# Kernel tuning notes

Hardware: AMD Instinct MI355X
Metric: run time of the kernel (lower is better)

Reference implementation:

```python
import jax, jax.numpy as jnp
import numpy as np

VOCAB_SIZE = 50000

def setup_inputs() -> dict:
    key = jax.random.key(0)
    # token index sequences: [batch, seq_len], values in [0, vocab)
    x = jax.random.randint(key, (2048, 200), 0, VOCAB_SIZE, dtype=jnp.int64)
    return {"x": x}

def reference(x) -> jnp.ndarray:
    # Faithful to: sum_{l} one_hot(x[b, l], V)  ->  [batch, vocab] count histogram.
    # Implemented as a scatter-add instead of materializing the
    # [batch, seq_len, vocab] one-hot tensor (same math, O(B*L) traffic on the
    # index side plus the [B, V] output).
    B, L = x.shape
    rows = jnp.broadcast_to(jnp.arange(B)[:, None], (B, L))  # [B, L]
    out = jnp.zeros((B, VOCAB_SIZE), dtype=jnp.float32)
    out = out.at[rows, x].add(jnp.float32(1.0))
    return out
```

## Files before the change

kernel.cpp:

```cpp
#include <hip/hip_runtime.h>
#include <hip/hip_bf16.h>

#define VOCAB 50000
#define SEQ   200
#define NDW   (VOCAB / 4)
#define NV4   (VOCAB / 16)

__global__ __launch_bounds__(256) void MultihotEmbedding_16458314678493_kernel(
    const int* __restrict__ x, float* __restrict__ out) {
  __shared__ unsigned cnt[NDW];

  uint4* __restrict__ c4 = (uint4*)cnt;
  const uint4 z = make_uint4(0u, 0u, 0u, 0u);
  for (int i = threadIdx.x; i < NV4; i += 256) c4[i] = z;
  __syncthreads();

  const int row = blockIdx.x;
  const int* __restrict__ xr = x + row * SEQ;
  for (int t = threadIdx.x; t < SEQ; t += 256) {
    const int idx = xr[t];
    atomicAdd(&cnt[idx >> 2], 1u << ((idx & 3) * 8));
  }
  __syncthreads();

  float4* __restrict__ o4 = (float4*)(out + (size_t)row * VOCAB);
  for (int i = threadIdx.x; i < NDW; i += 256) {
    const unsigned u = cnt[i];
    float4 v;
    v.x = (float)(u & 0xffu);
    v.y = (float)((u >> 8) & 0xffu);
    v.z = (float)((u >> 16) & 0xffu);
    v.w = (float)(u >> 24);
    o4[i] = v;
  }
}

extern "C" void kernel_launch(void* const* d_in, const int* in_sizes, int n_in,
                              void* d_out, int out_size, void* d_ws, size_t ws_size,
                              hipStream_t stream) {
  const int* x = (const int*)d_in[0];
  float* out = (float*)d_out;
  const int batch = in_sizes[0] / SEQ;
  MultihotEmbedding_16458314678493_kernel<<<batch, 256, 0, stream>>>(x, out);
}
```

Baseline: 406.3 us.

## Split each row's vocab into four chunks per block and use nontemporal stores

Each batch row is now handled by four blocks, each owning a quarter of the vocabulary with a smaller shared-memory histogram (about 12.5 KB instead of 50 KB). This lets more blocks fit on each CU and gives more parallelism for the write-bound output phase. Every block re-reads the row's 200 indices and skips those outside its range. Output stores become nontemporal to avoid polluting the cache with the large write stream.

After: 415.7 us. 2.3% more time.

```diff
diff --git a/kernel.cpp b/kernel.cpp
--- a/kernel.cpp
+++ b/kernel.cpp
@@ -1,37 +1,45 @@
 #include <hip/hip_runtime.h>
 #include <hip/hip_bf16.h>
 
-#define VOCAB 50000
-#define SEQ   200
-#define NDW   (VOCAB / 4)
-#define NV4   (VOCAB / 16)
+#define VOCAB   50000
+#define SEQ     200
+#define NCHUNK  4
+#define CHUNK   (VOCAB / NCHUNK)
+#define CDW     (CHUNK / 4)
+#define CDW_PAD 3136
+
+typedef float v4f __attribute__((ext_vector_type(4)));
+typedef unsigned v4u __attribute__((ext_vector_type(4)));
 
 __global__ __launch_bounds__(256) void MultihotEmbedding_16458314678493_kernel(
     const int* __restrict__ x, float* __restrict__ out) {
-  __shared__ unsigned cnt[NDW];
+  __shared__ unsigned cnt[CDW_PAD];
 
-  uint4* __restrict__ c4 = (uint4*)cnt;
-  const uint4 z = make_uint4(0u, 0u, 0u, 0u);
-  for (int i = threadIdx.x; i < NV4; i += 256) c4[i] = z;
+  v4u* __restrict__ c4 = (v4u*)cnt;
+  const v4u z = {0u, 0u, 0u, 0u};
+  for (int i = threadIdx.x; i < CDW_PAD / 4; i += 256) c4[i] = z;
   __syncthreads();
 
-  const int row = blockIdx.x;
+  const int row = blockIdx.x >> 2;
+  const int lo  = (blockIdx.x & 3) * CHUNK;
   const int* __restrict__ xr = x + row * SEQ;
+
   for (int t = threadIdx.x; t < SEQ; t += 256) {
-    const int idx = xr[t];
-    atomicAdd(&cnt[idx >> 2], 1u << ((idx & 3) * 8));
+    const int idx = xr[t] - lo;
+    if ((unsigned)idx < (unsigned)CHUNK)
+      atomicAdd(&cnt[idx >> 2], 1u << ((idx & 3) * 8));
   }
   __syncthreads();
 
-  float4* __restrict__ o4 = (float4*)(out + (size_t)row * VOCAB);
-  for (int i = threadIdx.x; i < NDW; i += 256) {
+  v4f* __restrict__ o4 = (v4f*)(out + (size_t)row * VOCAB + lo);
+  for (int i = threadIdx.x; i < CDW; i += 256) {
     const unsigned u = cnt[i];
-    float4 v;
+    v4f v;
     v.x = (float)(u & 0xffu);
     v.y = (float)((u >> 8) & 0xffu);
     v.z = (float)((u >> 16) & 0xffu);
     v.w = (float)(u >> 24);
-    o4[i] = v;
+    __builtin_nontemporal_store(v, &o4[i]);
   }
 }
 
@@ -41,5 +49,5 @@
   const int* x = (const int*)d_in[0];
   float* out = (float*)d_out;
   const int batch = in_sizes[0] / SEQ;
-  MultihotEmbedding_16458314678493_kernel<<<batch, 256, 0, stream>>>(x, out);
+  MultihotEmbedding_16458314678493_kernel<<<batch * NCHUNK, 256, 0, stream>>>(x, out);
 }
```
